# Performance work log

Hardware: AMD Instinct MI355X
Metric: run time of the kernel (lower is better)

The kernel has to match this reference:

```python
import math
import jax, jax.numpy as jnp
import numpy as np

B, H, S, D = 4, 16, 2048, 64
HEAD_DIM = 64

def setup_inputs() -> dict:
    key = jax.random.key(0)
    k1, k2, k3, k4 = jax.random.split(key, 4)
    return {
        "key": jax.random.normal(k1, (B, H, S, D), dtype=jnp.float32),
        "query": jax.random.normal(k2, (B, H, S, D), dtype=jnp.float32),
        "value": jax.random.normal(k3, (B, H, S, D), dtype=jnp.float32),
        "mask": jax.random.randint(k4, (1, 1, S, S), 0, 2) == 1,  # True = masked
    }

def reference(key, query, value, mask):
    # energy: [B, H, S, S]
    energy = jnp.einsum("bhqd,bhkd->bhqk", query, key)
    # faithful to torch: mask applied BEFORE scaling by 1/sqrt(head_dim)
    energy = jnp.where(mask, jnp.float32(-1e20), energy)
    attention_weight = jax.nn.softmax(energy / math.sqrt(HEAD_DIM), axis=-1)
    output = jnp.einsum("bhqk,bhkd->bhqd", attention_weight, value)
    return (output, attention_weight)
```

## Files before the change

kernel.cpp:

```cpp
#include <hip/hip_runtime.h>


namespace {
constexpr int Bn = 4, Hn = 16, Sn = 2048, Dn = 64;
constexpr int QB = 64;
constexpr int KT = 64;
constexpr int NIT = Sn / KT;
constexpr int NWG = (Sn / QB) * Hn * Bn;
}

using half8   = __attribute__((ext_vector_type(8))) _Float16;
using half4   = __attribute__((ext_vector_type(4))) _Float16;
using float4v = __attribute__((ext_vector_type(4))) float;
using int4v   = __attribute__((ext_vector_type(4))) int;

__device__ __forceinline__ half8 cvt_half8(float4v a, float4v b) {
    half8 f;
    f[0] = (_Float16)a[0]; f[1] = (_Float16)a[1];
    f[2] = (_Float16)a[2]; f[3] = (_Float16)a[3];
    f[4] = (_Float16)b[0]; f[5] = (_Float16)b[1];
    f[6] = (_Float16)b[2]; f[7] = (_Float16)b[3];
    return f;
}

__global__ __launch_bounds__(256, 4) void attn_fused(
    const float* __restrict__ Qg, const float* __restrict__ Kg,
    const float* __restrict__ Vg, const int* __restrict__ Mg,
    float* __restrict__ Og, float* __restrict__ Pg)
{
    __shared__ _Float16 Vt[Dn][KT + 8];
    __shared__ _Float16 Pt[QB][KT + 8];
    __shared__ float    lrow[QB];

    const int tid  = threadIdx.x;
    const int w    = tid >> 6;
    const int lane = tid & 63;
    const int c15  = lane & 15;
    const int q4   = lane >> 4;

    const int L    = blockIdx.x + (int)gridDim.x * (blockIdx.y + (int)gridDim.y * blockIdx.z);
    const int wid  = (L & 7) * (NWG / 8) + (L >> 3);
    const int qblk = wid & (Sn / QB - 1);
    const int h    = (wid / (Sn / QB)) & (Hn - 1);
    const int b    = wid / ((Sn / QB) * Hn);
    const int qbase = qblk * QB;

    const size_t headoff = ((size_t)(b * Hn + h)) * Sn * Dn;
    const float* Qh = Qg + headoff + (size_t)qbase * Dn;
    const float* Kh = Kg + headoff;
    const float* Vh = Vg + headoff;
    float*       Oh = Og + headoff + (size_t)qbase * Dn;
    const int* Mb = Mg + (size_t)(qbase + c15) * Sn + w * 16 + q4 * 4;
    float*     Pb = Pg + ((size_t)(b * Hn + h)) * Sn * Sn
                  + (size_t)(qbase + c15) * Sn + w * 16 + q4 * 4;

    if (tid < QB) lrow[tid] = 0.f;

    half8 qfr[8];
    #pragma unroll
    for (int m = 0; m < 4; ++m) {
        #pragma unroll
        for (int ks = 0; ks < 2; ++ks) {
            const float* p = Qh + (size_t)(m * 16 + c15) * Dn + ks * 32 + q4 * 8;
            qfr[m * 2 + ks] = cvt_half8(*(const float4v*)p, *(const float4v*)(p + 4));
        }
    }
    __syncthreads();

    const float* Kp = Kh + (size_t)(w * 16 + c15) * Dn + q4 * 8;
    float4v k0 = *(const float4v*)(Kp);
    float4v k1 = *(const float4v*)(Kp + 4);
    float4v k2 = *(const float4v*)(Kp + 32);
    float4v k3 = *(const float4v*)(Kp + 36);
    float lsum[4] = {0.f, 0.f, 0.f, 0.f};

    for (int t = 0; t < NIT; ++t) {
        const half8 a0 = cvt_half8(k0, k1);
        const half8 a1 = cvt_half8(k2, k3);
        if (t != NIT - 1) {
            Kp += KT * Dn;
            k0 = *(const float4v*)(Kp);
            k1 = *(const float4v*)(Kp + 4);
            k2 = *(const float4v*)(Kp + 32);
            k3 = *(const float4v*)(Kp + 36);
        }
        #pragma unroll
        for (int m = 0; m < 4; ++m) {
            const int4v mk = *(const int4v*)(Mb + (size_t)(m * 16) * Sn + t * KT);
            float4v D = {0.f, 0.f, 0.f, 0.f};
            D = __builtin_amdgcn_mfma_f32_16x16x32_f16(a0, qfr[2 * m + 0], D, 0, 0, 0);
            D = __builtin_amdgcn_mfma_f32_16x16x32_f16(a1, qfr[2 * m + 1], D, 0, 0, 0);
            lsum[m] += (mk[0] ? 0.f : __expf(D[0] * 0.125f))
                     + (mk[1] ? 0.f : __expf(D[1] * 0.125f))
                     + (mk[2] ? 0.f : __expf(D[2] * 0.125f))
                     + (mk[3] ? 0.f : __expf(D[3] * 0.125f));
        }
    }
    #pragma unroll
    for (int m = 0; m < 4; ++m) {
        lsum[m] += __shfl_xor(lsum[m], 16);
        lsum[m] += __shfl_xor(lsum[m], 32);
    }
    if (lane < 16) {
        #pragma unroll
        for (int m = 0; m < 4; ++m) atomicAdd(&lrow[m * 16 + lane], lsum[m]);
    }
    __syncthreads();
    if (tid < QB) lrow[tid] = 1.f / lrow[tid];
    __syncthreads();
    float linv[4];
    #pragma unroll
    for (int m = 0; m < 4; ++m) linv[m] = lrow[m * 16 + c15];

    float4v Of[4];
    #pragma unroll
    for (int m = 0; m < 4; ++m) Of[m] = {0.f, 0.f, 0.f, 0.f};

    Kp = Kh + (size_t)(w * 16 + c15) * Dn + q4 * 8;
    k0 = *(const float4v*)(Kp);
    k1 = *(const float4v*)(Kp + 4);
    k2 = *(const float4v*)(Kp + 32);
    k3 = *(const float4v*)(Kp + 36);

    const int vr = tid >> 4;
    const int vc = (tid & 15) << 2;
    const float* Vp = Vh + (size_t)vr * Dn + vc;
    float4v v0 = *(const float4v*)(Vp);
    float4v v1 = *(const float4v*)(Vp + 16 * Dn);
    float4v v2 = *(const float4v*)(Vp + 32 * Dn);
    float4v v3 = *(const float4v*)(Vp + 48 * Dn);

    #pragma unroll 1
    for (int t = 0; t < NIT; ++t) {
        const half8 a0 = cvt_half8(k0, k1);
        const half8 a1 = cvt_half8(k2, k3);
        if (t != NIT - 1) {
            Kp += KT * Dn;
            k0 = *(const float4v*)(Kp);
            k1 = *(const float4v*)(Kp + 4);
            k2 = *(const float4v*)(Kp + 32);
            k3 = *(const float4v*)(Kp + 36);
        }
        half4 ph0, ph1, ph2, ph3;
        #pragma unroll
        for (int m = 0; m < 4; ++m) {
            const int4v mk = *(const int4v*)(Mb + (size_t)(m * 16) * Sn + t * KT);
            float4v D = {0.f, 0.f, 0.f, 0.f};
            D = __builtin_amdgcn_mfma_f32_16x16x32_f16(a0, qfr[2 * m + 0], D, 0, 0, 0);
            D = __builtin_amdgcn_mfma_f32_16x16x32_f16(a1, qfr[2 * m + 1], D, 0, 0, 0);
            float4v pw;
            pw[0] = mk[0] ? 0.f : __expf(D[0] * 0.125f) * linv[m];
            pw[1] = mk[1] ? 0.f : __expf(D[1] * 0.125f) * linv[m];
            pw[2] = mk[2] ? 0.f : __expf(D[2] * 0.125f) * linv[m];
            pw[3] = mk[3] ? 0.f : __expf(D[3] * 0.125f) * linv[m];
            __builtin_nontemporal_store(pw, (float4v*)(Pb + (size_t)(m * 16) * Sn + t * KT));
            half4 hp;
            hp[0] = (_Float16)pw[0]; hp[1] = (_Float16)pw[1];
            hp[2] = (_Float16)pw[2]; hp[3] = (_Float16)pw[3];
            if (m == 0) ph0 = hp; else if (m == 1) ph1 = hp;
            else if (m == 2) ph2 = hp; else ph3 = hp;
        }
        __syncthreads();
        *(half4*)&Pt[ 0 + c15][w * 16 + q4 * 4] = ph0;
        *(half4*)&Pt[16 + c15][w * 16 + q4 * 4] = ph1;
        *(half4*)&Pt[32 + c15][w * 16 + q4 * 4] = ph2;
        *(half4*)&Pt[48 + c15][w * 16 + q4 * 4] = ph3;
        Vt[vc + 0][vr +  0] = (_Float16)v0[0];
        Vt[vc + 1][vr +  0] = (_Float16)v0[1];
        Vt[vc + 2][vr +  0] = (_Float16)v0[2];
        Vt[vc + 3][vr +  0] = (_Float16)v0[3];
        Vt[vc + 0][vr + 16] = (_Float16)v1[0];
        Vt[vc + 1][vr + 16] = (_Float16)v1[1];
        Vt[vc + 2][vr + 16] = (_Float16)v1[2];
        Vt[vc + 3][vr + 16] = (_Float16)v1[3];
        Vt[vc + 0][vr + 32] = (_Float16)v2[0];
        Vt[vc + 1][vr + 32] = (_Float16)v2[1];
        Vt[vc + 2][vr + 32] = (_Float16)v2[2];
        Vt[vc + 3][vr + 32] = (_Float16)v2[3];
        Vt[vc + 0][vr + 48] = (_Float16)v3[0];
        Vt[vc + 1][vr + 48] = (_Float16)v3[1];
        Vt[vc + 2][vr + 48] = (_Float16)v3[2];
        Vt[vc + 3][vr + 48] = (_Float16)v3[3];
        if (t != NIT - 1) {
            const float* Vn = Vp + (size_t)(t + 1) * KT * Dn;
            v0 = *(const float4v*)(Vn);
            v1 = *(const float4v*)(Vn + 16 * Dn);
            v2 = *(const float4v*)(Vn + 32 * Dn);
            v3 = *(const float4v*)(Vn + 48 * Dn);
        }
        __syncthreads();
        #pragma unroll
        for (int ks = 0; ks < 2; ++ks) {
            const half8 bv = *(const half8*)&Vt[w * 16 + c15][ks * 32 + q4 * 8];
            Of[0] = __builtin_amdgcn_mfma_f32_16x16x32_f16(
                        *(const half8*)&Pt[ 0 + c15][ks * 32 + q4 * 8], bv, Of[0], 0, 0, 0);
            Of[1] = __builtin_amdgcn_mfma_f32_16x16x32_f16(
                        *(const half8*)&Pt[16 + c15][ks * 32 + q4 * 8], bv, Of[1], 0, 0, 0);
            Of[2] = __builtin_amdgcn_mfma_f32_16x16x32_f16(
                        *(const half8*)&Pt[32 + c15][ks * 32 + q4 * 8], bv, Of[2], 0, 0, 0);
            Of[3] = __builtin_amdgcn_mfma_f32_16x16x32_f16(
                        *(const half8*)&Pt[48 + c15][ks * 32 + q4 * 8], bv, Of[3], 0, 0, 0);
        }
    }

    #pragma unroll
    for (int m = 0; m < 4; ++m) {
        #pragma unroll
        for (int r = 0; r < 4; ++r) {
            Oh[(size_t)(m * 16 + q4 * 4 + r) * Dn + w * 16 + c15] = Of[m][r];
        }
    }
}

extern "C" void kernel_launch(void* const* d_in, const int* in_sizes, int n_in,
                              void* d_out, int out_size, void* d_ws, size_t ws_size,
                              hipStream_t stream) {
    (void)in_sizes; (void)n_in; (void)d_ws; (void)ws_size; (void)out_size;
    const float* Kg = (const float*)d_in[0];
    const float* Qg = (const float*)d_in[1];
    const float* Vg = (const float*)d_in[2];
    const int*   Mg = (const int*)d_in[3];
    float* Og = (float*)d_out;
    float* Pg = Og + (size_t)Bn * Hn * Sn * Dn;
    dim3 grid(Sn / QB, Hn, Bn), block(256);
    attn_fused<<<grid, block, 0, stream>>>(Qg, Kg, Vg, Mg, Og, Pg);
}
```

Baseline: 1.629 ms.

## Bit-pack mask, compute PV from registers, reduce output across waves in LDS

A pre-pass kernel packs the int mask into 64-bit ballot words, cutting per-tile mask reads from int4 loads to a single u64 per row. The second pass no longer stages P and V through shared memory with two barriers per tile. Each wave instead feeds its own P fragment and directly loaded V values into 16x16x16 MFMAs, producing partial outputs over its key slice. These partials are summed across the four waves with LDS atomics at the end. The cost is 64 accumulator registers, uncoalesced scalar V loads, no K/V prefetch and lower occupancy (launch bounds 3).

Measured after the change: 1.741 ms. +6.9%, slower.

```diff
diff --git a/kernel.cpp b/kernel.cpp
--- a/kernel.cpp
+++ b/kernel.cpp
@@ -7,12 +7,13 @@
 constexpr int KT = 64;
 constexpr int NIT = Sn / KT;
 constexpr int NWG = (Sn / QB) * Hn * Bn;
+constexpr int MW  = Sn / 64;
 }
 
 using half8   = __attribute__((ext_vector_type(8))) _Float16;
 using half4   = __attribute__((ext_vector_type(4))) _Float16;
 using float4v = __attribute__((ext_vector_type(4))) float;
-using int4v   = __attribute__((ext_vector_type(4))) int;
+typedef unsigned long long u64;
 
 __device__ __forceinline__ half8 cvt_half8(float4v a, float4v b) {
     half8 f;
@@ -23,20 +24,30 @@
     return f;
 }
 
-__global__ __launch_bounds__(256, 4) void attn_fused(
+__global__ __launch_bounds__(256) void mask_pack(const int* __restrict__ Mg,
+                                                 u64* __restrict__ Wb)
+{
+    const int gw   = (blockIdx.x * 256 + threadIdx.x) >> 6;
+    const int lane = threadIdx.x & 63;
+    const int row  = gw >> 5, wi = gw & 31;
+    const u64 bal  = __ballot(Mg[(size_t)row * Sn + wi * 64 + lane] != 0);
+    if (lane == 0) Wb[(size_t)row * MW + wi] = bal;
+}
+
+__global__ __launch_bounds__(256, 3) void attn_fused(
     const float* __restrict__ Qg, const float* __restrict__ Kg,
-    const float* __restrict__ Vg, const int* __restrict__ Mg,
+    const float* __restrict__ Vg, const u64* __restrict__ Wb,
     float* __restrict__ Og, float* __restrict__ Pg)
 {
-    __shared__ _Float16 Vt[Dn][KT + 8];
-    __shared__ _Float16 Pt[QB][KT + 8];
-    __shared__ float    lrow[QB];
+    __shared__ float lrow[QB];
+    __shared__ float Olds[QB][68];
 
     const int tid  = threadIdx.x;
     const int w    = tid >> 6;
     const int lane = tid & 63;
     const int c15  = lane & 15;
     const int q4   = lane >> 4;
+    const int sh   = w * 16 + q4 * 4;
 
     const int L    = blockIdx.x + (int)gridDim.x * (blockIdx.y + (int)gridDim.y * blockIdx.z);
     const int wid  = (L & 7) * (NWG / 8) + (L >> 3);
@@ -50,9 +61,9 @@
     const float* Kh = Kg + headoff;
     const float* Vh = Vg + headoff;
     float*       Oh = Og + headoff + (size_t)qbase * Dn;
-    const int* Mb = Mg + (size_t)(qbase + c15) * Sn + w * 16 + q4 * 4;
-    float*     Pb = Pg + ((size_t)(b * Hn + h)) * Sn * Sn
-                  + (size_t)(qbase + c15) * Sn + w * 16 + q4 * 4;
+    const u64*   Mb = Wb + (size_t)(qbase + c15) * MW;
+    float*       Pb = Pg + ((size_t)(b * Hn + h)) * Sn * Sn
+                    + (size_t)(qbase + c15) * Sn + sh;
 
     if (tid < QB) lrow[tid] = 0.f;
 
@@ -85,143 +96,126 @@
             k3 = *(const float4v*)(Kp + 36);
         }
         #pragma unroll
-        for (int m = 0; m < 4; ++m) {
-            const int4v mk = *(const int4v*)(Mb + (size_t)(m * 16) * Sn + t * KT);
+        for (int mb = 0; mb < 4; ++mb) {
+            const u64 ms = Mb[(size_t)(mb * 16) * MW + t] >> sh;
             float4v D = {0.f, 0.f, 0.f, 0.f};
-            D = __builtin_amdgcn_mfma_f32_16x16x32_f16(a0, qfr[2 * m + 0], D, 0, 0, 0);
-            D = __builtin_amdgcn_mfma_f32_16x16x32_f16(a1, qfr[2 * m + 1], D, 0, 0, 0);
-            lsum[m] += (mk[0] ? 0.f : __expf(D[0] * 0.125f))
-                     + (mk[1] ? 0.f : __expf(D[1] * 0.125f))
-                     + (mk[2] ? 0.f : __expf(D[2] * 0.125f))
-                     + (mk[3] ? 0.f : __expf(D[3] * 0.125f));
-        }
-    }
-    #pragma unroll
-    for (int m = 0; m < 4; ++m) {
-        lsum[m] += __shfl_xor(lsum[m], 16);
-        lsum[m] += __shfl_xor(lsum[m], 32);
+            D = __builtin_amdgcn_mfma_f32_16x16x32_f16(a0, qfr[2 * mb + 0], D, 0, 0, 0);
+            D = __builtin_amdgcn_mfma_f32_16x16x32_f16(a1, qfr[2 * mb + 1], D, 0, 0, 0);
+            lsum[mb] += ((ms      & 1) ? 0.f : __expf(D[0] * 0.125f))
+                      + ((ms >> 1 & 1) ? 0.f : __expf(D[1] * 0.125f))
+                      + ((ms >> 2 & 1) ? 0.f : __expf(D[2] * 0.125f))
+                      + ((ms >> 3 & 1) ? 0.f : __expf(D[3] * 0.125f));
+        }
+    }
+    #pragma unroll
+    for (int mb = 0; mb < 4; ++mb) {
+        lsum[mb] += __shfl_xor(lsum[mb], 16);
+        lsum[mb] += __shfl_xor(lsum[mb], 32);
     }
     if (lane < 16) {
         #pragma unroll
-        for (int m = 0; m < 4; ++m) atomicAdd(&lrow[m * 16 + lane], lsum[m]);
+        for (int mb = 0; mb < 4; ++mb) atomicAdd(&lrow[mb * 16 + lane], lsum[mb]);
     }
     __syncthreads();
     if (tid < QB) lrow[tid] = 1.f / lrow[tid];
     __syncthreads();
     float linv[4];
     #pragma unroll
-    for (int m = 0; m < 4; ++m) linv[m] = lrow[m * 16 + c15];
-
-    float4v Of[4];
-    #pragma unroll
-    for (int m = 0; m < 4; ++m) Of[m] = {0.f, 0.f, 0.f, 0.f};
-
-    Kp = Kh + (size_t)(w * 16 + c15) * Dn + q4 * 8;
-    k0 = *(const float4v*)(Kp);
-    k1 = *(const float4v*)(Kp + 4);
-    k2 = *(const float4v*)(Kp + 32);
-    k3 = *(const float4v*)(Kp + 36);
-
-    const int vr = tid >> 4;
-    const int vc = (tid & 15) << 2;
-    const float* Vp = Vh + (size_t)vr * Dn + vc;
-    float4v v0 = *(const float4v*)(Vp);
-    float4v v1 = *(const float4v*)(Vp + 16 * Dn);
-    float4v v2 = *(const float4v*)(Vp + 32 * Dn);
-    float4v v3 = *(const float4v*)(Vp + 48 * Dn);
+    for (int mb = 0; mb < 4; ++mb) linv[mb] = lrow[mb * 16 + c15];
+
+    float4v Of[16];
+    #pragma unroll
+    for (int i = 0; i < 16; ++i) Of[i] = {0.f, 0.f, 0.f, 0.f};
+
+    const float* Vb0 = Vh + (size_t)(w * 16 + q4 * 4) * Dn + c15;
 
     #pragma unroll 1
     for (int t = 0; t < NIT; ++t) {
-        const half8 a0 = cvt_half8(k0, k1);
-        const half8 a1 = cvt_half8(k2, k3);
-        if (t != NIT - 1) {
-            Kp += KT * Dn;
-            k0 = *(const float4v*)(Kp);
-            k1 = *(const float4v*)(Kp + 4);
-            k2 = *(const float4v*)(Kp + 32);
-            k3 = *(const float4v*)(Kp + 36);
-        }
+        const float* Kt = Kh + (size_t)(t * KT + w * 16 + c15) * Dn + q4 * 8;
+        const float4v kk0 = *(const float4v*)(Kt);
+        const float4v kk1 = *(const float4v*)(Kt + 4);
+        const float4v kk2 = *(const float4v*)(Kt + 32);
+        const float4v kk3 = *(const float4v*)(Kt + 36);
+        const float* Vt = Vb0 + (size_t)t * KT * Dn;
+        float v[16];
+        #pragma unroll
+        for (int j = 0; j < 4; ++j)
+            #pragma unroll
+            for (int db = 0; db < 4; ++db)
+                v[j * 4 + db] = Vt[j * Dn + db * 16];
+        u64 ms[4];
+        #pragma unroll
+        for (int mb = 0; mb < 4; ++mb) ms[mb] = Mb[(size_t)(mb * 16) * MW + t] >> sh;
+
+        const half8 a0 = cvt_half8(kk0, kk1);
+        const half8 a1 = cvt_half8(kk2, kk3);
         half4 ph0, ph1, ph2, ph3;
         #pragma unroll
-        for (int m = 0; m < 4; ++m) {
-            const int4v mk = *(const int4v*)(Mb + (size_t)(m * 16) * Sn + t * KT);
+        for (int mb = 0; mb < 4; ++mb) {
             float4v D = {0.f, 0.f, 0.f, 0.f};
-            D = __builtin_amdgcn_mfma_f32_16x16x32_f16(a0, qfr[2 * m + 0], D, 0, 0, 0);
-            D = __builtin_amdgcn_mfma_f32_16x16x32_f16(a1, qfr[2 * m + 1], D, 0, 0, 0);
+            D = __builtin_amdgcn_mfma_f32_16x16x32_f16(a0, qfr[2 * mb + 0], D, 0, 0, 0);
+            D = __builtin_amdgcn_mfma_f32_16x16x32_f16(a1, qfr[2 * mb + 1], D, 0, 0, 0);
             float4v pw;
-            pw[0] = mk[0] ? 0.f : __expf(D[0] * 0.125f) * linv[m];
-            pw[1] = mk[1] ? 0.f : __expf(D[1] * 0.125f) * linv[m];
-            pw[2] = mk[2] ? 0.f : __expf(D[2] * 0.125f) * linv[m];
-            pw[3] = mk[3] ? 0.f : __expf(D[3] * 0.125f) * linv[m];
-            __builtin_nontemporal_store(pw, (float4v*)(Pb + (size_t)(m * 16) * Sn + t * KT));
+            pw[0] = (ms[mb]      & 1) ? 0.f : __expf(D[0] * 0.125f) * linv[mb];
+            pw[1] = (ms[mb] >> 1 & 1) ? 0.f : __expf(D[1] * 0.125f) * linv[mb];
+            pw[2] = (ms[mb] >> 2 & 1) ? 0.f : __expf(D[2] * 0.125f) * linv[mb];
+            pw[3] = (ms[mb] >> 3 & 1) ? 0.f : __expf(D[3] * 0.125f) * linv[mb];
+            __builtin_nontemporal_store(pw,
+                (float4v*)(Pb + (size_t)(mb * 16) * Sn + t * KT));
             half4 hp;
             hp[0] = (_Float16)pw[0]; hp[1] = (_Float16)pw[1];
             hp[2] = (_Float16)pw[2]; hp[3] = (_Float16)pw[3];
-            if (m == 0) ph0 = hp; else if (m == 1) ph1 = hp;
-            else if (m == 2) ph2 = hp; else ph3 = hp;
-        }
-        __syncthreads();
-        *(half4*)&Pt[ 0 + c15][w * 16 + q4 * 4] = ph0;
-        *(half4*)&Pt[16 + c15][w * 16 + q4 * 4] = ph1;
-        *(half4*)&Pt[32 + c15][w * 16 + q4 * 4] = ph2;
-        *(half4*)&Pt[48 + c15][w * 16 + q4 * 4] = ph3;
-        Vt[vc + 0][vr +  0] = (_Float16)v0[0];
-        Vt[vc + 1][vr +  0] = (_Float16)v0[1];
-        Vt[vc + 2][vr +  0] = (_Float16)v0[2];
-        Vt[vc + 3][vr +  0] = (_Float16)v0[3];
-        Vt[vc + 0][vr + 16] = (_Float16)v1[0];
-        Vt[vc + 1][vr + 16] = (_Float16)v1[1];
-        Vt[vc + 2][vr + 16] = (_Float16)v1[2];
-        Vt[vc + 3][vr + 16] = (_Float16)v1[3];
-        Vt[vc + 0][vr + 32] = (_Float16)v2[0];
-        Vt[vc + 1][vr + 32] = (_Float16)v2[1];
-        Vt[vc + 2][vr + 32] = (_Float16)v2[2];
-        Vt[vc + 3][vr + 32] = (_Float16)v2[3];
-        Vt[vc + 0][vr + 48] = (_Float16)v3[0];
-        Vt[vc + 1][vr + 48] = (_Float16)v3[1];
-        Vt[vc + 2][vr + 48] = (_Float16)v3[2];
-        Vt[vc + 3][vr + 48] = (_Float16)v3[3];
-        if (t != NIT - 1) {
-            const float* Vn = Vp + (size_t)(t + 1) * KT * Dn;
-            v0 = *(const float4v*)(Vn);
-            v1 = *(const float4v*)(Vn + 16 * Dn);
-            v2 = *(const float4v*)(Vn + 32 * Dn);
-            v3 = *(const float4v*)(Vn + 48 * Dn);
-        }
-        __syncthreads();
-        #pragma unroll
-        for (int ks = 0; ks < 2; ++ks) {
-            const half8 bv = *(const half8*)&Vt[w * 16 + c15][ks * 32 + q4 * 8];
-            Of[0] = __builtin_amdgcn_mfma_f32_16x16x32_f16(
-                        *(const half8*)&Pt[ 0 + c15][ks * 32 + q4 * 8], bv, Of[0], 0, 0, 0);
-            Of[1] = __builtin_amdgcn_mfma_f32_16x16x32_f16(
-                        *(const half8*)&Pt[16 + c15][ks * 32 + q4 * 8], bv, Of[1], 0, 0, 0);
-            Of[2] = __builtin_amdgcn_mfma_f32_16x16x32_f16(
-                        *(const half8*)&Pt[32 + c15][ks * 32 + q4 * 8], bv, Of[2], 0, 0, 0);
-            Of[3] = __builtin_amdgcn_mfma_f32_16x16x32_f16(
-                        *(const half8*)&Pt[48 + c15][ks * 32 + q4 * 8], bv, Of[3], 0, 0, 0);
-        }
-    }
-
-    #pragma unroll
-    for (int m = 0; m < 4; ++m) {
-        #pragma unroll
-        for (int r = 0; r < 4; ++r) {
-            Oh[(size_t)(m * 16 + q4 * 4 + r) * Dn + w * 16 + c15] = Of[m][r];
-        }
+            if (mb == 0) ph0 = hp; else if (mb == 1) ph1 = hp;
+            else if (mb == 2) ph2 = hp; else ph3 = hp;
+        }
+        #pragma unroll
+        for (int db = 0; db < 4; ++db) {
+            half4 bf;
+            bf[0] = (_Float16)v[ 0 + db];
+            bf[1] = (_Float16)v[ 4 + db];
+            bf[2] = (_Float16)v[ 8 + db];
+            bf[3] = (_Float16)v[12 + db];
+            Of[0 * 4 + db] = __builtin_amdgcn_mfma_f32_16x16x16f16(ph0, bf, Of[0 * 4 + db], 0, 0, 0);
+            Of[1 * 4 + db] = __builtin_amdgcn_mfma_f32_16x16x16f16(ph1, bf, Of[1 * 4 + db], 0, 0, 0);
+            Of[2 * 4 + db] = __builtin_amdgcn_mfma_f32_16x16x16f16(ph2, bf, Of[2 * 4 + db], 0, 0, 0);
+            Of[3 * 4 + db] = __builtin_amdgcn_mfma_f32_16x16x16f16(ph3, bf, Of[3 * 4 + db], 0, 0, 0);
+        }
+    }
+
+    __syncthreads();
+    for (int i = tid; i < QB * 68; i += 256) ((float*)Olds)[i] = 0.f;
+    __syncthreads();
+    #pragma unroll
+    for (int mb = 0; mb < 4; ++mb)
+        #pragma unroll
+        for (int db = 0; db < 4; ++db)
+            #pragma unroll
+            for (int r = 0; r < 4; ++r)
+                atomicAdd(&Olds[mb * 16 + q4 * 4 + r][db * 16 + c15],
+                          Of[mb * 4 + db][r]);
+    __syncthreads();
+    const int orow = tid >> 2, ocol = (tid & 3) << 4;
+    #pragma unroll
+    for (int cc = 0; cc < 16; cc += 4) {
+        *(float4v*)(Oh + (size_t)orow * Dn + ocol + cc) =
+            *(const float4v*)&Olds[orow][ocol + cc];
     }
 }
 
 extern "C" void kernel_launch(void* const* d_in, const int* in_sizes, int n_in,
                               void* d_out, int out_size, void* d_ws, size_t ws_size,
                               hipStream_t stream) {
-    (void)in_sizes; (void)n_in; (void)d_ws; (void)ws_size; (void)out_size;
+    (void)in_sizes; (void)n_in; (void)ws_size; (void)out_size;
     const float* Kg = (const float*)d_in[0];
     const float* Qg = (const float*)d_in[1];
     const float* Vg = (const float*)d_in[2];
     const int*   Mg = (const int*)d_in[3];
     float* Og = (float*)d_out;
     float* Pg = Og + (size_t)Bn * Hn * Sn * Dn;
+    u64*   Wb = (u64*)d_ws;
+
+    mask_pack<<<dim3(Sn * MW / 4), dim3(256), 0, stream>>>(Mg, Wb);
+
     dim3 grid(Sn / QB, Hn, Bn), block(256);
-    attn_fused<<<grid, block, 0, stream>>>(Qg, Kg, Vg, Mg, Og, Pg);
-}
+    attn_fused<<<grid, block, 0, stream>>>(Qg, Kg, Vg, Wb, Og, Pg);
+}
```
